# Performance work log

Hardware: AMD Instinct MI355X
Metric: run time of the kernel (lower is better)

## Reference

```python
import jax, jax.numpy as jnp
import numpy as np

B, D, H = 2048, 1024, 16
DH = D // H            # 64 head dim
R = DH // 2            # 32 random-feature dim (kernel_type has no 'northogonal')
EPS = 1e-3             # keras LayerNormalization default epsilon


def _orthogonal(seed):
    # mirrors random_orthogonal(shape=(1,H,1,DH,R)): QR of flat (H*DH, R) matrix
    rng = np.random.default_rng(seed)
    a = rng.standard_normal((H * DH, R)).astype(np.float32)
    q, r = np.linalg.qr(a)
    q = q * np.sign(np.diag(r))[None, :]
    return jnp.asarray(q.reshape(H, DH, R))


def setup_inputs() -> dict:
    key = jax.random.key(0)
    ks = jax.random.split(key, 8)
    inp = {
        "x": jax.random.normal(ks[0], (B, D), jnp.float32),
        # states start as small positive values so den = phi4(q) . new_z > 0
        "s": jax.random.uniform(ks[1], (B, D * R), jnp.float32),
        "z": jax.random.uniform(ks[2], (B, R * H), jnp.float32),
        "ln1_g": jnp.ones((D,), jnp.float32),
        "ln1_b": jnp.zeros((D,), jnp.float32),
        "ln2_g": jnp.ones((D,), jnp.float32),
        "ln2_b": jnp.zeros((D,), jnp.float32),
        "W_attn": jax.random.normal(ks[3], (D, 3 * D), jnp.float32) * 0.02,
        "b_attn": jnp.zeros((3 * D,), jnp.float32),
        "W_proj": jax.random.normal(ks[4], (D, D), jnp.float32) * 0.02,
        "b_proj": jnp.zeros((D,), jnp.float32),
        "W_fc": jax.random.normal(ks[5], (D, 4 * D), jnp.float32) * 0.02,
        "b_fc": jnp.zeros((4 * D,), jnp.float32),
        "W_mp": jax.random.normal(ks[6], (4 * D, D), jnp.float32) * 0.02,
        "b_mp": jnp.zeros((D,), jnp.float32),
    }
    for i in range(4):
        inp[f"w{i + 1}"] = _orthogonal(100 + i)
    return inp


def _ln(x, g, b):
    m = jnp.mean(x, axis=-1, keepdims=True)
    v = jnp.var(x, axis=-1, keepdims=True)
    return g * (x - m) * jax.lax.rsqrt(v + EPS) + b


def _phi(x, w):
    # x: [B,H,dh], w: [H,dh,R] orthogonal random features; kernel 'sigmoid'
    return jax.nn.sigmoid(jnp.einsum('bhd,hdr->bhr', x, w))


def reference(x, s, z, ln1_g, ln1_b, ln2_g, ln2_b, W_attn, b_attn,
              W_proj, b_proj, W_fc, b_fc, W_mp, b_mp, w1, w2, w3, w4):
    bsz = x.shape[0]
    h1 = _ln(x, ln1_g, ln1_b)
    qkv = h1 @ W_attn + b_attn                      # [B, 3D]
    q, k, v = jnp.split(qkv, 3, axis=1)
    q = q.reshape(bsz, H, DH)
    k = k.reshape(bsz, H, DH)
    v = v.reshape(bsz, H, DH)
    s4 = s.reshape(bsz, H, R, DH)
    z3 = z.reshape(bsz, H, R)
    # kernelized linear-attention state update (outer-product accumulation)
    new_s = s4 + jnp.einsum('bhr,bhd->bhrd', _phi(k, w1), v)   # [B,H,R,DH]
    new_z = z3 + _phi(k, w2)                                   # [B,H,R]
    num = jnp.einsum('bhr,bhrd->bhd', _phi(q, w3), new_s)      # [B,H,DH]
    den = jnp.einsum('bhr,bhr->bh', _phi(q, w4), new_z)[..., None]
    head = (num / den).reshape(bsz, D)
    attention = head @ W_proj + b_proj
    h2 = _ln(attention + x, ln2_g, ln2_b)          # dropout: inference mode
    ffn = jax.nn.gelu(h2 @ W_fc + b_fc, approximate=False) @ W_mp + b_mp
    out = h2 + ffn
    return out, new_s.reshape(bsz, D * R), new_z.reshape(bsz, R * H)
```

## Files before the change

kernel.cpp:

```cpp
#include <hip/hip_runtime.h>
#include <hip/hip_bf16.h>
#include <math.h>


#define Bsz 2048
#define Dm  1024
#define Hh  16
#define DHd 64
#define Rr  32

typedef __bf16 bf16x8 __attribute__((ext_vector_type(8)));
typedef __bf16 bf16x4 __attribute__((ext_vector_type(4)));
typedef float  f32x4  __attribute__((ext_vector_type(4)));

__device__ __forceinline__ __bf16 f2bf(float x) { return (__bf16)x; }

#define GLOAD_LDS16(g, l) __builtin_amdgcn_global_load_lds(               \
    (const __attribute__((address_space(1))) void*)(g),                   \
    (__attribute__((address_space(3))) void*)(l), 16, 0, 0)

__global__ __launch_bounds__(256) void wtrans_kernel(
    const float* __restrict__ W, __bf16* __restrict__ Wt, int K, int N)
{
  __shared__ float tile[32][33];
  const int tx = threadIdx.x & 31;
  const int ty0 = threadIdx.x >> 5;
  const int bn = blockIdx.x * 32;
  const int bk = blockIdx.y * 32;
#pragma unroll
  for (int j = 0; j < 4; ++j)
    tile[ty0 + j * 8][tx] = W[(size_t)(bk + ty0 + j * 8) * N + bn + tx];
  __syncthreads();
#pragma unroll
  for (int j = 0; j < 4; ++j) {
    const int ny = ty0 + j * 8;
    Wt[(size_t)(bn + ny) * K + bk + tx] = f2bf(tile[tx][ny]);
  }
}

template<bool ADD, typename TA>
__global__ __launch_bounds__(256) void ln_kernel(
    const TA* __restrict__ a, const float* __restrict__ b2,
    const float* __restrict__ g, const float* __restrict__ beta,
    __bf16* __restrict__ outb, float* __restrict__ outf)
{
  const int row = blockIdx.x;
  const int t = threadIdx.x;
  const size_t base = (size_t)row * Dm;
  float vals[4];
#pragma unroll
  for (int i = 0; i < 4; ++i) {
    const int c = t * 4 + i;
    float v = (float)a[base + c];
    if (ADD) v += b2[base + c];
    vals[i] = v;
  }
  float sm = 0.f, sq = 0.f;
#pragma unroll
  for (int i = 0; i < 4; ++i) { sm += vals[i]; sq += vals[i] * vals[i]; }
  for (int off = 32; off > 0; off >>= 1) {
    sm += __shfl_down(sm, off);
    sq += __shfl_down(sq, off);
  }
  __shared__ float smw[4], sqw[4];
  if ((t & 63) == 0) { smw[t >> 6] = sm; sqw[t >> 6] = sq; }
  __syncthreads();
  const float S  = smw[0] + smw[1] + smw[2] + smw[3];
  const float SS = sqw[0] + sqw[1] + sqw[2] + sqw[3];
  const float mean = S * (1.f / Dm);
  const float var  = SS * (1.f / Dm) - mean * mean;
  const float inv  = rsqrtf(var + 1e-3f);
#pragma unroll
  for (int i = 0; i < 4; ++i) {
    const int c = t * 4 + i;
    const float r = g[c] * ((vals[i] - mean) * inv) + beta[c];
    outb[base + c] = f2bf(r);
    if (ADD) outf[base + c] = r;
  }
}

template<int BM, int BN, bool GELU, bool RES, bool OUTF32, bool SPLITK2>
__global__ __launch_bounds__(256) void gemm_kernel(
    const __bf16* __restrict__ A, const __bf16* __restrict__ Bt,
    const float* __restrict__ bias, const float* __restrict__ res,
    void* __restrict__ Cv, int M, int N, int K)
{
  constexpr int FM = BM / 32;
  constexpr int FN = BN / 32;
  constexpr int LPS = BM / 64 + BN / 64;
  __shared__ __align__(16) __bf16 lsA[2][BM * 32];
  __shared__ __align__(16) __bf16 lsB[2][BN * 32];
  const int t = threadIdx.x;
  const int wave = t >> 6, lane = t & 63;
  const int quad = lane >> 4, l16 = lane & 15;
  const int wm = wave >> 1, wn = wave & 1;
  const int bm = blockIdx.x * BM, bn = blockIdx.y * BN;
  const int kHalf = SPLITK2 ? K / 2 : K;
  const int k0 = SPLITK2 ? blockIdx.z * kHalf : 0;
  const int nt = kHalf / 32;

  const int srow = lane >> 2, scol = (lane & 3) * 8;
  const __bf16* Ag = A  + (size_t)(bm + wave * 16 + srow) * K + scol;
  const __bf16* Bg = Bt + (size_t)(bn + wave * 16 + srow) * K + scol;

  f32x4 acc[FM][FN];
#pragma unroll
  for (int mi = 0; mi < FM; ++mi)
#pragma unroll
    for (int ni = 0; ni < FN; ++ni)
      acc[mi][ni] = (f32x4){0.f, 0.f, 0.f, 0.f};

  auto STAGE = [&](int buf, int kt) {
#pragma unroll
    for (int i = 0; i < BM / 64; ++i)
      GLOAD_LDS16(Ag + (size_t)(i * 64) * K + kt,
                  &lsA[buf][(i * 64 + wave * 16) * 32]);
#pragma unroll
    for (int i = 0; i < BN / 64; ++i)
      GLOAD_LDS16(Bg + (size_t)(i * 64) * K + kt,
                  &lsB[buf][(i * 64 + wave * 16) * 32]);
  };
  auto COMPUTE = [&](int buf) {
    bf16x8 af[FM], bfr[FN];
#pragma unroll
    for (int mi = 0; mi < FM; ++mi)
      af[mi] = *(const bf16x8*)
          &lsA[buf][(wm * (BM / 2) + mi * 16 + l16) * 32 + quad * 8];
#pragma unroll
    for (int ni = 0; ni < FN; ++ni)
      bfr[ni] = *(const bf16x8*)
          &lsB[buf][(wn * (BN / 2) + ni * 16 + l16) * 32 + quad * 8];
#pragma unroll
    for (int mi = 0; mi < FM; ++mi)
#pragma unroll
      for (int ni = 0; ni < FN; ++ni)
        acc[mi][ni] = __builtin_amdgcn_mfma_f32_16x16x32_bf16(
            af[mi], bfr[ni], acc[mi][ni], 0, 0, 0);
  };

  STAGE(0, k0);
  STAGE(1, k0 + 32);
  asm volatile("s_waitcnt vmcnt(%0)" :: "i"(LPS) : "memory");
  __builtin_amdgcn_sched_barrier(0);
  __builtin_amdgcn_s_barrier();

  for (int tt = 0; tt < nt; ++tt) {
    const int buf = tt & 1;
    COMPUTE(buf);
    __builtin_amdgcn_sched_barrier(0);
    __builtin_amdgcn_s_barrier();
    const int knext = k0 + 32 * (tt + 2 < nt ? tt + 2 : nt - 1);
    STAGE(buf, knext);
    asm volatile("s_waitcnt vmcnt(%0)" :: "i"(LPS) : "memory");
    __builtin_amdgcn_sched_barrier(0);
    __builtin_amdgcn_s_barrier();
  }

#pragma unroll
  for (int mi = 0; mi < FM; ++mi) {
    const int row0 = bm + wm * (BM / 2) + mi * 16 + quad * 4;
#pragma unroll
    for (int ni = 0; ni < FN; ++ni) {
      const int col = bn + wn * (BN / 2) + ni * 16 + l16;
      const float bv = SPLITK2 ? 0.f : bias[col];
#pragma unroll
      for (int i = 0; i < 4; ++i) {
        const int row = row0 + i;
        float v = acc[mi][ni][i] + bv;
        if (SPLITK2) {
          ((float*)Cv)[(size_t)blockIdx.z * M * N + (size_t)row * N + col] = v;
        } else {
          if (GELU) v = 0.5f * v * (1.0f + erff(v * 0.70710678118654752f));
          if (RES) v += res[(size_t)row * N + col];
          if (OUTF32) ((float*)Cv)[(size_t)row * N + col] = v;
          else        ((__bf16*)Cv)[(size_t)row * N + col] = f2bf(v);
        }
      }
    }
  }
}

__global__ __launch_bounds__(256) void reduce_mp_kernel(
    const float* __restrict__ p, const float* __restrict__ bias,
    const float* __restrict__ res, float* __restrict__ out)
{
  const size_t i = ((size_t)blockIdx.x * 256 + threadIdx.x) * 4;
  const f32x4 a = *(const f32x4*)(p + i);
  const f32x4 b = *(const f32x4*)(p + (size_t)Bsz * Dm + i);
  const f32x4 r = *(const f32x4*)(res + i);
  const f32x4 bv = *(const f32x4*)(bias + (i & (Dm - 1)));
  *(f32x4*)(out + i) = a + b + r + bv;
}

__global__ __launch_bounds__(256) void attn_kernel(
    const float* __restrict__ qkv, const float* __restrict__ s,
    const float* __restrict__ z,
    const float* __restrict__ w1, const float* __restrict__ w2,
    const float* __restrict__ w3, const float* __restrict__ w4,
    float* __restrict__ new_s, float* __restrict__ new_z,
    __bf16* __restrict__ head)
{
  const int wave = threadIdx.x >> 6, lane = threadIdx.x & 63;
  const int bh = blockIdx.x * 4 + wave;
  const int b = bh >> 4, h = bh & 15;
  __shared__ float ksh[4][64], qsh[4][64], vsh[4][64];
  __shared__ float phish[4][4][32];
  __shared__ float nzsh[4][32];

  const float* qrow = qkv + (size_t)b * (3 * Dm) + h * 64 + lane;
  qsh[wave][lane] = qrow[0];
  ksh[wave][lane] = qrow[Dm];
  vsh[wave][lane] = qrow[2 * Dm];
  __syncthreads();

  {
    const int r = lane & 31;
    for (int it = 0; it < 2; ++it) {
      const int mm = (lane >> 5) + it * 2;
      const float* wp = (mm == 0) ? w1 : (mm == 1) ? w2 : (mm == 2) ? w3 : w4;
      const float* w = wp + (size_t)h * (DHd * Rr) + r;
      const float* src = (it == 0) ? ksh[wave] : qsh[wave];
      float acc = 0.f;
#pragma unroll 8
      for (int d = 0; d < 64; ++d) acc += src[d] * w[(size_t)d * 32];
      phish[wave][mm][r] = 1.f / (1.f + expf(-acc));
    }
  }
  __syncthreads();

  const size_t zbase = (size_t)b * (Rr * Hh) + h * Rr;
  if (lane < 32) {
    const float nz = z[zbase + lane] + phish[wave][1][lane];
    new_z[zbase + lane] = nz;
    nzsh[wave][lane] = nz;
  }
  __syncthreads();

  float den = 0.f;
#pragma unroll
  for (int r = 0; r < 32; ++r) den += phish[wave][3][r] * nzsh[wave][r];

  const size_t sbase = ((size_t)b * Hh + h) * (Rr * DHd);
  const int d4 = (lane & 15) * 4, rr = lane >> 4;
  const f32x4 vv4 = *(const f32x4*)&vsh[wave][d4];
  f32x4 num4 = {0.f, 0.f, 0.f, 0.f};
#pragma unroll
  for (int rb = 0; rb < 8; ++rb) {
    const int r = rb * 4 + rr;
    f32x4 sv = *(const f32x4*)(s + sbase + r * 64 + d4);
    const f32x4 ns = sv + phish[wave][0][r] * vv4;
    *(f32x4*)(new_s + sbase + r * 64 + d4) = ns;
    num4 += phish[wave][2][r] * ns;
  }
#pragma unroll
  for (int i = 0; i < 4; ++i) {
    num4[i] += __shfl_xor(num4[i], 16);
    num4[i] += __shfl_xor(num4[i], 32);
  }
  if (rr == 0) {
    const float inv = 1.f / den;
    bf16x4 hv;
#pragma unroll
    for (int i = 0; i < 4; ++i) hv[i] = f2bf(num4[i] * inv);
    *(bf16x4*)(head + (size_t)b * Dm + h * 64 + d4) = hv;
  }
}

extern "C" void kernel_launch(void* const* d_in, const int* in_sizes, int n_in,
                              void* d_out, int out_size, void* d_ws, size_t ws_size,
                              hipStream_t stream)
{
  const float* x      = (const float*)d_in[0];
  const float* s_in   = (const float*)d_in[1];
  const float* z_in   = (const float*)d_in[2];
  const float* ln1_g  = (const float*)d_in[3];
  const float* ln1_b  = (const float*)d_in[4];
  const float* ln2_g  = (const float*)d_in[5];
  const float* ln2_b  = (const float*)d_in[6];
  const float* W_attn = (const float*)d_in[7];
  const float* b_attn = (const float*)d_in[8];
  const float* W_proj = (const float*)d_in[9];
  const float* b_proj = (const float*)d_in[10];
  const float* W_fc   = (const float*)d_in[11];
  const float* b_fc   = (const float*)d_in[12];
  const float* W_mp   = (const float*)d_in[13];
  const float* b_mp   = (const float*)d_in[14];
  const float* w1     = (const float*)d_in[15];
  const float* w2     = (const float*)d_in[16];
  const float* w3     = (const float*)d_in[17];
  const float* w4     = (const float*)d_in[18];

  float* out0  = (float*)d_out;
  float* out_s = out0 + (size_t)Bsz * Dm;
  float* out_z = out_s + (size_t)Bsz * Dm * Rr;

  char* ws = (char*)d_ws;
  __bf16* h1    = (__bf16*)(ws);
  float*  qkv   = (float*) (ws + ((size_t)4  << 20));
  __bf16* headp = (__bf16*)(ws + ((size_t)28 << 20));
  __bf16* attnb = (__bf16*)(ws + ((size_t)32 << 20));
  __bf16* h2b   = (__bf16*)(ws + ((size_t)36 << 20));
  float*  h2f   = (float*) (ws + ((size_t)40 << 20));
  __bf16* fcb   = (__bf16*)(ws + ((size_t)48 << 20));
  __bf16* Wt_attn = (__bf16*)(ws + ((size_t)48 << 20));
  __bf16* Wt_proj = (__bf16*)(ws + ((size_t)54 << 20));
  __bf16* Wt_fc   = (__bf16*)(ws + ((size_t)4  << 20));
  __bf16* Wt_mp   = (__bf16*)(ws + ((size_t)12 << 20));
  float*  mp_part = (float*) (ws + ((size_t)20 << 20));

  wtrans_kernel<<<dim3((3 * Dm) / 32, Dm / 32), 256, 0, stream>>>(
      W_attn, Wt_attn, Dm, 3 * Dm);
  wtrans_kernel<<<dim3(Dm / 32, Dm / 32), 256, 0, stream>>>(
      W_proj, Wt_proj, Dm, Dm);

  ln_kernel<false, float><<<Bsz, 256, 0, stream>>>(
      x, nullptr, ln1_g, ln1_b, h1, nullptr);
  gemm_kernel<128, 128, false, false, true, false>
      <<<dim3(Bsz / 128, (3 * Dm) / 128), 256, 0, stream>>>(
      h1, Wt_attn, b_attn, nullptr, qkv, Bsz, 3 * Dm, Dm);
  attn_kernel<<<Bsz * Hh / 4, 256, 0, stream>>>(qkv, s_in, z_in, w1, w2, w3, w4,
                                                out_s, out_z, headp);

  wtrans_kernel<<<dim3((4 * Dm) / 32, Dm / 32), 256, 0, stream>>>(
      W_fc, Wt_fc, Dm, 4 * Dm);
  wtrans_kernel<<<dim3(Dm / 32, (4 * Dm) / 32), 256, 0, stream>>>(
      W_mp, Wt_mp, 4 * Dm, Dm);

  gemm_kernel<64, 64, false, false, false, false>
      <<<dim3(Bsz / 64, Dm / 64), 256, 0, stream>>>(
      headp, Wt_proj, b_proj, nullptr, attnb, Bsz, Dm, Dm);
  ln_kernel<true, __bf16><<<Bsz, 256, 0, stream>>>(
      attnb, x, ln2_g, ln2_b, h2b, h2f);
  gemm_kernel<128, 128, true, false, false, false>
      <<<dim3(Bsz / 128, (4 * Dm) / 128), 256, 0, stream>>>(
      h2b, Wt_fc, b_fc, nullptr, fcb, Bsz, 4 * Dm, Dm);
  gemm_kernel<128, 64, false, false, true, true>
      <<<dim3(Bsz / 128, Dm / 64, 2), 256, 0, stream>>>(
      fcb, Wt_mp, nullptr, nullptr, mp_part, Bsz, Dm, 4 * Dm);
  reduce_mp_kernel<<<(Bsz * Dm) / (256 * 4), 256, 0, stream>>>(
      mp_part, b_mp, h2f, out0);
}
```

Baseline: 678.3 us.

## Share per-head feature weights in LDS across batches and swizzle GEMM tile order

The attention kernel now assigns one head per block, with each of the four waves handling a different batch row. This lets the block load the four random-feature matrices for that head once into padded LDS, instead of every wave reading them strided from global memory. Separately, the GEMM remaps its workgroup IDs so consecutive blocks are spread in groups of eight, which may improve L2/XCD locality across the chiplets. The LDS footprint grows by about 33KB per block, which can lower occupancy, and the swizzle assumes the block count is divisible by 8.

Result: faster. 664.2 us (-2.1%).

```diff
diff --git a/kernel.cpp b/kernel.cpp
--- a/kernel.cpp
+++ b/kernel.cpp
@@ -94,7 +94,13 @@
   const int wave = t >> 6, lane = t & 63;
   const int quad = lane >> 4, l16 = lane & 15;
   const int wm = wave >> 1, wn = wave & 1;
-  const int bm = blockIdx.x * BM, bn = blockIdx.y * BN;
+
+  int wg = blockIdx.y * gridDim.x + blockIdx.x;
+  const int nwg = gridDim.x * gridDim.y;
+  const int cpx = nwg >> 3;
+  wg = (wg & 7) * cpx + (wg >> 3);
+  const int bm = (wg % gridDim.x) * BM, bn = (wg / gridDim.x) * BN;
+
   const int kHalf = SPLITK2 ? K / 2 : K;
   const int k0 = SPLITK2 ? blockIdx.z * kHalf : 0;
   const int nt = kHalf / 32;
@@ -201,12 +207,25 @@
     __bf16* __restrict__ head)
 {
   const int wave = threadIdx.x >> 6, lane = threadIdx.x & 63;
-  const int bh = blockIdx.x * 4 + wave;
-  const int b = bh >> 4, h = bh & 15;
+  const int h = blockIdx.x & 15;
+  const int b = (blockIdx.x >> 4) * 4 + wave;
+  __shared__ float wl[4][Rr][65];
   __shared__ float ksh[4][64], qsh[4][64], vsh[4][64];
   __shared__ float phish[4][4][32];
   __shared__ float nzsh[4][32];
 
+  {
+    const float* wp = (wave == 0) ? w1 : (wave == 1) ? w2 : (wave == 2) ? w3 : w4;
+    const float* wh = wp + (size_t)h * (DHd * Rr);
+#pragma unroll
+    for (int j = 0; j < 8; ++j) {
+      const int e = lane * 4 + j * 256;
+      const f32x4 v = *(const f32x4*)(wh + e);
+      const int d = e >> 5, r0 = e & 31;
+#pragma unroll
+      for (int q = 0; q < 4; ++q) wl[wave][r0 + q][d] = v[q];
+    }
+  }
   const float* qrow = qkv + (size_t)b * (3 * Dm) + h * 64 + lane;
   qsh[wave][lane] = qrow[0];
   ksh[wave][lane] = qrow[Dm];
@@ -215,14 +234,14 @@
 
   {
     const int r = lane & 31;
+    const int half = lane >> 5;
     for (int it = 0; it < 2; ++it) {
-      const int mm = (lane >> 5) + it * 2;
-      const float* wp = (mm == 0) ? w1 : (mm == 1) ? w2 : (mm == 2) ? w3 : w4;
-      const float* w = wp + (size_t)h * (DHd * Rr) + r;
+      const int mm = half + it * 2;
+      const float* wr = &wl[mm][r][0];
       const float* src = (it == 0) ? ksh[wave] : qsh[wave];
       float acc = 0.f;
 #pragma unroll 8
-      for (int d = 0; d < 64; ++d) acc += src[d] * w[(size_t)d * 32];
+      for (int d = 0; d < 64; ++d) acc += src[d] * wr[d];
       phish[wave][mm][r] = 1.f / (1.f + expf(-acc));
     }
   }
```
